# Performance work log

Hardware: AMD Instinct MI355X
Metric: run time of the kernel (lower is better)

Reference implementation:

```python
import jax, jax.numpy as jnp
import numpy as np

N = 4096   # query tokens
M = 4096   # key/value tokens
D = 512    # embedding_dim


def setup_inputs() -> dict:
    key = jax.random.key(0)
    kq, kk, kv = jax.random.split(key, 3)
    return {
        "query": jax.random.normal(kq, (N, D), dtype=jnp.float32),
        "key": jax.random.normal(kk, (M, D), dtype=jnp.float32),
        "value": jax.random.normal(kv, (M, D), dtype=jnp.float32),
    }


def reference(query, key, value):
    # scores = Q K^T  (no 1/sqrt(d) scaling in the original module)
    attention_scores = jnp.einsum("nd,md->nm", query, key)  # [N, M]
    attention_probs = jax.nn.softmax(attention_scores, axis=-1)  # [N, M]
    output = jnp.einsum("nm,md->nd", attention_probs, value)  # [N, D]
    return (output, attention_probs)
```

## Files before the change

kernel.cpp:

```cpp
#include <hip/hip_runtime.h>
#include <hip/hip_bf16.h>
#include <stdint.h>

#define N_Q 4096
#define N_K 4096
#define DIM 512

typedef float f32x4 __attribute__((ext_vector_type(4)));
typedef __bf16 bf16x8 __attribute__((ext_vector_type(8)));
typedef unsigned short u16x4 __attribute__((ext_vector_type(4)));
typedef int i32x4 __attribute__((ext_vector_type(4)));

__device__ __forceinline__ f32x4 mfma_bf16(bf16x8 a, bf16x8 b, f32x4 c) {
  return __builtin_amdgcn_mfma_f32_16x16x32_bf16(a, b, c, 0, 0, 0);
}

__device__ __forceinline__ i32x4 mfma_i8(i32x4 a, i32x4 b, i32x4 c) {
  return __builtin_amdgcn_mfma_i32_16x16x64_i8(a, b, c, 0, 0, 0);
}

__device__ __forceinline__ void gload16(const void* g, void* l) {
  __builtin_amdgcn_global_load_lds((const __attribute__((address_space(1))) void*)g,
                                   (__attribute__((address_space(3))) void*)l,
                                   16, 0, 0);
}

__device__ __forceinline__ void split4(const f32x4 v, u16x4& h, u16x4& l) {
#pragma unroll
  for (int i = 0; i < 4; ++i) {
    float f = v[i];
    uint32_t u = __builtin_bit_cast(uint32_t, f);
    uint32_t hb = (u + 0x8000u) & 0xffff0000u;
    float hf = __builtin_bit_cast(float, hb);
    float lf = f - hf;
    h[i] = (unsigned short)(hb >> 16);
    l[i] = (unsigned short)(__builtin_bit_cast(uint32_t, lf) >> 16);
  }
}

__device__ __forceinline__ unsigned short bf16r(float f) {
  uint32_t u = __builtin_bit_cast(uint32_t, f);
  return (unsigned short)((u + 0x8000u) >> 16);
}

__global__ __launch_bounds__(256) void prep_kernel(const float* __restrict__ Q,
                                                   const float* __restrict__ K,
                                                   const float* __restrict__ V,
                                                   signed char* __restrict__ Xq8,
                                                   signed char* __restrict__ Xk8,
                                                   float* __restrict__ sclA,
                                                   float* __restrict__ sclB,
                                                   unsigned short* __restrict__ Vt) {
  __shared__ unsigned short t[64][72];
  const int bid = blockIdx.x;
  const int tid = threadIdx.x;

  if (bid < 2048) {
    const bool isK = bid >= 1024;
    const float* X = isK ? K : Q;
    signed char* X8 = isK ? Xk8 : Xq8;
    float* scl = isK ? sclB : sclA;
    const int lane = tid & 63;
    const int row = (isK ? bid - 1024 : bid) * 4 + (tid >> 6);

    f32x4 v[2];
    v[0] = *(const f32x4*)(X + (size_t)row * DIM + lane * 8);
    v[1] = *(const f32x4*)(X + (size_t)row * DIM + lane * 8 + 4);

    float mx = 0.f;
#pragma unroll
    for (int u = 0; u < 2; ++u)
#pragma unroll
      for (int j = 0; j < 4; ++j) mx = fmaxf(mx, fabsf(v[u][j]));
#pragma unroll
    for (int o = 32; o > 0; o >>= 1) mx = fmaxf(mx, __shfl_xor(mx, o, 64));

    const float s = fmaxf(mx, 1e-20f) * (1.0f / 127.0f);
    const float rinv = 1.0f / s;
    const float linv = 128.0f * rinv;

    uint32_t hw[2], lw[2];
#pragma unroll
    for (int u = 0; u < 2; ++u) {
      uint32_t hword = 0, lword = 0;
#pragma unroll
      for (int j = 0; j < 4; ++j) {
        float x = v[u][j];
        int h = __float2int_rn(x * rinv);
        float r = x - s * (float)h;
        int l = __float2int_rn(r * linv);
        hword |= ((uint32_t)(h & 0xff)) << (8 * j);
        lword |= ((uint32_t)(l & 0xff)) << (8 * j);
      }
      hw[u] = hword; lw[u] = lword;
    }
    uint2 hv; hv.x = hw[0]; hv.y = hw[1];
    uint2 lv; lv.x = lw[0]; lv.y = lw[1];
    *(uint2*)(X8 + (size_t)row * 1024 + lane * 8) = hv;
    *(uint2*)(X8 + (size_t)row * 1024 + 512 + lane * 8) = lv;
    if (lane == 0) scl[row] = s;
  } else {
    const int b2 = bid - 2048;
    const int d0 = (b2 & 7) * 64;
    const int k0 = (b2 >> 3) * 64;
#pragma unroll
    for (int c = 0; c < 4; ++c) {
      int kr = (tid >> 4) + c * 16;
      f32x4 v = *(const f32x4*)(V + (size_t)(k0 + kr) * DIM + d0 + (tid & 15) * 4);
#pragma unroll
      for (int j = 0; j < 4; ++j) t[(tid & 15) * 4 + j][kr] = bf16r(v[j]);
    }
    __syncthreads();
#pragma unroll
    for (int c = 0; c < 2; ++c) {
      int d = (tid >> 3) + c * 32;
      int k = (tid & 7) * 8;
      *(uint4*)(Vt + (size_t)(d0 + d) * N_K + k0 + k) = *(const uint4*)&t[d][k];
    }
  }
}

__global__ __launch_bounds__(512, 2) void qk5_kernel(const signed char* __restrict__ Xq8,
                                                     const signed char* __restrict__ Xk8,
                                                     const float* __restrict__ sclA,
                                                     const float* __restrict__ sclB,
                                                     float* __restrict__ S) {
  __shared__ __align__(16) char smem[98304];

  const int tid = threadIdx.x;
  const int lane = tid & 63, wid = tid >> 6;
  const int wr = wid >> 1, wc = wid & 1;

  const int bid = blockIdx.x;
  const int b = (bid & 7) * 64 + (bid >> 3);
  const int rbase = (b >> 5) * 256;
  const int cbase = (b & 31) * 128;

  const i32x4 izero = {0, 0, 0, 0};
  i32x4 acc_hh[4][4], acc_x[4][4];
#pragma unroll
  for (int m = 0; m < 4; ++m)
#pragma unroll
    for (int n = 0; n < 4; ++n) { acc_hh[m][n] = izero; acc_x[m][n] = izero; }

  auto stage = [&](int buf, int t) {
    const int rsub = tid >> 3;
    const int sc = (lane & 7) ^ ((lane >> 3) & 7);
    const int colb = (sc < 4) ? (t * 64 + sc * 16) : (512 + t * 64 + (sc & 3) * 16);
#pragma unroll
    for (int i = 0; i < 4; ++i) {
      const int r = i * 64 + rsub;
      const signed char* g = Xq8 + (size_t)(rbase + r) * 1024 + colb;
      uint32_t off = (uint32_t)(buf * 49152 + ((i * 64 + wid * 8) << 7));
      off = (uint32_t)__builtin_amdgcn_readfirstlane((int)off);
      gload16(g, smem + off);
    }
#pragma unroll
    for (int i = 0; i < 2; ++i) {
      const int r = i * 64 + rsub;
      const signed char* g = Xk8 + (size_t)(cbase + r) * 1024 + colb;
      uint32_t off = (uint32_t)(buf * 49152 + 32768 + ((i * 64 + wid * 8) << 7));
      off = (uint32_t)__builtin_amdgcn_readfirstlane((int)off);
      gload16(g, smem + off);
    }
  };

  auto compute = [&](int buf) {
    const char* bA = smem + buf * 49152;
    const char* bB = bA + 32768;
    const int kc = lane >> 4;
    i32x4 ah[4], al[4], bh[4], bl[4];
#pragma unroll
    for (int m = 0; m < 4; ++m) {
      int row = (wr << 6) + (m << 4) + (lane & 15);
      ah[m] = *(const i32x4*)(bA + row * 128 + ((kc ^ (row & 7)) << 4));
      al[m] = *(const i32x4*)(bA + row * 128 + (((4 + kc) ^ (row & 7)) << 4));
    }
#pragma unroll
    for (int n = 0; n < 4; ++n) {
      int row = (wc << 6) + (n << 4) + (lane & 15);
      bh[n] = *(const i32x4*)(bB + row * 128 + ((kc ^ (row & 7)) << 4));
      bl[n] = *(const i32x4*)(bB + row * 128 + (((4 + kc) ^ (row & 7)) << 4));
    }
    __builtin_amdgcn_s_setprio(1);
#pragma unroll
    for (int m = 0; m < 4; ++m)
#pragma unroll
      for (int n = 0; n < 4; ++n) {
        acc_hh[m][n] = mfma_i8(ah[m], bh[n], acc_hh[m][n]);
        acc_x[m][n]  = mfma_i8(ah[m], bl[n], acc_x[m][n]);
        acc_x[m][n]  = mfma_i8(al[m], bh[n], acc_x[m][n]);
      }
    __builtin_amdgcn_s_setprio(0);
  };

  stage(0, 0);
  stage(1, 1);
  for (int t = 0; t < 8; ++t) {
    if (t < 7) asm volatile("s_waitcnt vmcnt(6)" ::: "memory");
    else       asm volatile("s_waitcnt vmcnt(0)" ::: "memory");
    __builtin_amdgcn_s_barrier();
    compute(t & 1);
    asm volatile("s_waitcnt lgkmcnt(0)" ::: "memory");
    __builtin_amdgcn_sched_barrier(0);
    __builtin_amdgcn_s_barrier();
    if (t + 2 < 8) stage(t & 1, t + 2);
  }

#pragma unroll
  for (int m = 0; m < 4; ++m) {
    int row0 = rbase + wr * 64 + m * 16 + (lane >> 4) * 4;
    float sa[4];
#pragma unroll
    for (int j = 0; j < 4; ++j) sa[j] = sclA[row0 + j];
#pragma unroll
    for (int n = 0; n < 4; ++n) {
      int col = cbase + wc * 64 + n * 16 + (lane & 15);
      float sb = sclB[col];
#pragma unroll
      for (int j = 0; j < 4; ++j) {
        float f = (float)acc_hh[m][n][j] + (float)acc_x[m][n][j] * 0.0078125f;
        S[(size_t)(row0 + j) * N_K + col] = sa[j] * sb * f;
      }
    }
  }
}

__global__ __launch_bounds__(256, 2) void qk_kernel(const float* __restrict__ Q,
                                                    const float* __restrict__ K,
                                                    float* __restrict__ S) {
  __shared__ __align__(16) char sAh[16384];
  __shared__ __align__(16) char sAl[16384];
  __shared__ __align__(16) char sBh[16384];
  __shared__ __align__(16) char sBl[16384];

  const int tid = threadIdx.x;
  const int rbase = blockIdx.y * 128;
  const int cbase = blockIdx.x * 128;
  const int lane = tid & 63, wid = tid >> 6;
  const int wr = wid >> 1, wc = wid & 1;
  const int lr = lane & 15, lk = (lane >> 4) * 8;

  const int srow = tid >> 4;
  const int scol = (tid & 15) * 4;

  f32x4 qr[8], kr[8];
#pragma unroll
  for (int p = 0; p < 8; ++p) {
    int r = p * 16 + srow;
    qr[p] = *(const f32x4*)(Q + (size_t)(rbase + r) * DIM + scol);
    kr[p] = *(const f32x4*)(K + (size_t)(cbase + r) * DIM + scol);
  }

  const f32x4 fzero = {0.f, 0.f, 0.f, 0.f};
  f32x4 acc[4][4];
#pragma unroll
  for (int m = 0; m < 4; ++m)
#pragma unroll
    for (int n = 0; n < 4; ++n) acc[m][n] = fzero;

  for (int kk = 0; kk < DIM / 64; ++kk) {
    __syncthreads();
#pragma unroll
    for (int p = 0; p < 8; ++p) {
      int r = p * 16 + srow;
      uint32_t bo = (uint32_t)(r * 128) + (uint32_t)((scol * 2) ^ ((r & 7) << 4));
      u16x4 qh, ql, kh, kl;
      split4(qr[p], qh, ql);
      split4(kr[p], kh, kl);
      *(u16x4*)(sAh + bo) = qh;
      *(u16x4*)(sAl + bo) = ql;
      *(u16x4*)(sBh + bo) = kh;
      *(u16x4*)(sBl + bo) = kl;
    }
    __syncthreads();
    if (kk < DIM / 64 - 1) {
#pragma unroll
      for (int p = 0; p < 8; ++p) {
        int r = p * 16 + srow;
        qr[p] = *(const f32x4*)(Q + (size_t)(rbase + r) * DIM + (kk + 1) * 64 + scol);
        kr[p] = *(const f32x4*)(K + (size_t)(cbase + r) * DIM + (kk + 1) * 64 + scol);
      }
    }
#pragma unroll
    for (int kh = 0; kh < 2; ++kh) {
      bf16x8 a_h[4], a_l[4], b_h[4], b_l[4];
#pragma unroll
      for (int m = 0; m < 4; ++m) {
        int row = wr * 64 + m * 16 + lr;
        uint32_t co = (uint32_t)(((kh * 32 + lk) * 2) ^ ((row & 7) << 4));
        a_h[m] = *(const bf16x8*)(sAh + row * 128 + co);
        a_l[m] = *(const bf16x8*)(sAl + row * 128 + co);
      }
#pragma unroll
      for (int n = 0; n < 4; ++n) {
        int row = wc * 64 + n * 16 + lr;
        uint32_t co = (uint32_t)(((kh * 32 + lk) * 2) ^ ((row & 7) << 4));
        b_h[n] = *(const bf16x8*)(sBh + row * 128 + co);
        b_l[n] = *(const bf16x8*)(sBl + row * 128 + co);
      }
#pragma unroll
      for (int m = 0; m < 4; ++m)
#pragma unroll
        for (int n = 0; n < 4; ++n) {
          acc[m][n] = mfma_bf16(a_h[m], b_h[n], acc[m][n]);
          acc[m][n] = mfma_bf16(a_h[m], b_l[n], acc[m][n]);
          acc[m][n] = mfma_bf16(a_l[m], b_h[n], acc[m][n]);
        }
    }
  }

#pragma unroll
  for (int m = 0; m < 4; ++m) {
    int row = rbase + wr * 64 + m * 16 + (lane >> 4) * 4;
#pragma unroll
    for (int n = 0; n < 4; ++n) {
      int col = cbase + wc * 64 + n * 16 + lr;
#pragma unroll
      for (int j = 0; j < 4; ++j)
        S[(size_t)(row + j) * N_K + col] = acc[m][n][j];
    }
  }
}

__global__ __launch_bounds__(256) void softmax_kernel(float* __restrict__ P,
                                                      unsigned short* __restrict__ Pb) {
  const int tid = threadIdx.x;
  const int wid = tid >> 6, lane = tid & 63;
  float* p = P + (size_t)blockIdx.x * N_K;

  f32x4 v[4];
  float mx = -3.0e38f;
#pragma unroll
  for (int i = 0; i < 4; ++i) {
    v[i] = *(const f32x4*)(p + i * 1024 + tid * 4);
    mx = fmaxf(mx, fmaxf(fmaxf(v[i][0], v[i][1]), fmaxf(v[i][2], v[i][3])));
  }
#pragma unroll
  for (int o = 32; o > 0; o >>= 1) mx = fmaxf(mx, __shfl_xor(mx, o, 64));
  __shared__ float redM[4];
  __shared__ float redS[4];
  if (lane == 0) redM[wid] = mx;
  __syncthreads();
  mx = fmaxf(fmaxf(redM[0], redM[1]), fmaxf(redM[2], redM[3]));

  float s = 0.f;
#pragma unroll
  for (int i = 0; i < 4; ++i) {
#pragma unroll
    for (int j = 0; j < 4; ++j) {
      v[i][j] = __expf(v[i][j] - mx);
      s += v[i][j];
    }
  }
#pragma unroll
  for (int o = 32; o > 0; o >>= 1) s += __shfl_xor(s, o, 64);
  if (lane == 0) redS[wid] = s;
  __syncthreads();
  s = redS[0] + redS[1] + redS[2] + redS[3];
  const float inv = 1.0f / s;

  unsigned short* pb = Pb + (size_t)blockIdx.x * N_K;
#pragma unroll
  for (int i = 0; i < 4; ++i) {
    v[i] *= inv;
    *(f32x4*)(p + i * 1024 + tid * 4) = v[i];
    u16x4 h;
#pragma unroll
    for (int j = 0; j < 4; ++j) h[j] = bf16r(v[i][j]);
    *(u16x4*)(pb + i * 1024 + tid * 4) = h;
  }
}

__global__ __launch_bounds__(256, 2) void pv5_kernel(const unsigned short* __restrict__ Pb,
                                                     const unsigned short* __restrict__ Vt,
                                                     float* __restrict__ Opart) {
  __shared__ __align__(16) char smem[65536];

  const int tid = threadIdx.x;
  const int lane = tid & 63, wid = tid >> 6;
  const int wr = wid >> 1, wc = wid & 1;
  const int rbase = blockIdx.y * 128;
  const int cbase = blockIdx.x * 128;
  const int k0 = blockIdx.z * 1024;
  float* Out = Opart + (size_t)blockIdx.z * ((size_t)N_Q * DIM);

  const int lrow = lane >> 3;
  const int lchk = lane & 7;

  const f32x4 fzero = {0.f, 0.f, 0.f, 0.f};
  f32x4 acc[4][4];
#pragma unroll
  for (int m = 0; m < 4; ++m)
#pragma unroll
    for (int n = 0; n < 4; ++n) acc[m][n] = fzero;

  auto stage = [&](int buf, int t) {
    const size_t kel = (size_t)k0 + ((size_t)t << 6);
#pragma unroll
    for (int i = 0; i < 4; ++i) {
      const int rr = (wid << 5) + (i << 3) + lrow;
      const int gc = lchk ^ (rr & 7);
      const void* gA = (const void*)(Pb + (size_t)(rbase + rr) * N_K + kel + (gc << 3));
      uint32_t off = (uint32_t)(buf * 32768 + (((wid << 5) + (i << 3)) << 7));
      off = (uint32_t)__builtin_amdgcn_readfirstlane((int)off);
      gload16(gA, smem + off);
    }
#pragma unroll
    for (int i = 0; i < 4; ++i) {
      const int rr = (wid << 5) + (i << 3) + lrow;
      const int gc = lchk ^ (rr & 7);
      const void* gB = (const void*)(Vt + (size_t)(cbase + rr) * N_K + kel + (gc << 3));
      uint32_t off = (uint32_t)(buf * 32768 + 16384 + (((wid << 5) + (i << 3)) << 7));
      off = (uint32_t)__builtin_amdgcn_readfirstlane((int)off);
      gload16(gB, smem + off);
    }
  };

  auto compute = [&](int buf) {
    const char* bA = smem + buf * 32768;
    const char* bB = bA + 16384;
#pragma unroll
    for (int kh = 0; kh < 2; ++kh) {
      bf16x8 a[4], bfr[4];
#pragma unroll
      for (int m = 0; m < 4; ++m) {
        int row = (wr << 6) + (m << 4) + (lane & 15);
        uint32_t co = (uint32_t)(((((kh << 2) + (lane >> 4)) << 4)) ^ ((row & 7) << 4));
        a[m] = *(const bf16x8*)(bA + row * 128 + co);
      }
#pragma unroll
      for (int n = 0; n < 4; ++n) {
        int row = (wc << 6) + (n << 4) + (lane & 15);
        uint32_t co = (uint32_t)(((((kh << 2) + (lane >> 4)) << 4)) ^ ((row & 7) << 4));
        bfr[n] = *(const bf16x8*)(bB + row * 128 + co);
      }
      __builtin_amdgcn_s_setprio(1);
#pragma unroll
      for (int m = 0; m < 4; ++m)
#pragma unroll
        for (int n = 0; n < 4; ++n)
          acc[m][n] = mfma_bf16(a[m], bfr[n], acc[m][n]);
      __builtin_amdgcn_s_setprio(0);
    }
  };

  stage(0, 0);
  stage(1, 1);
  for (int t = 0; t < 16; ++t) {
    if (t < 15) asm volatile("s_waitcnt vmcnt(8)" ::: "memory");
    else        asm volatile("s_waitcnt vmcnt(0)" ::: "memory");
    __builtin_amdgcn_s_barrier();
    compute(t & 1);
    asm volatile("s_waitcnt lgkmcnt(0)" ::: "memory");
    __builtin_amdgcn_sched_barrier(0);
    __builtin_amdgcn_s_barrier();
    if (t + 2 < 16) stage(t & 1, t + 2);
  }

#pragma unroll
  for (int m = 0; m < 4; ++m) {
    int row = rbase + wr * 64 + m * 16 + (lane >> 4) * 4;
#pragma unroll
    for (int n = 0; n < 4; ++n) {
      int col = cbase + wc * 64 + n * 16 + (lane & 15);
#pragma unroll
      for (int j = 0; j < 4; ++j)
        Out[(size_t)(row + j) * DIM + col] = acc[m][n][j];
    }
  }
}

__global__ __launch_bounds__(256) void reduce_kernel(float* __restrict__ O,
                                                     const float* __restrict__ Opart) {
  size_t i = ((size_t)blockIdx.x * 256 + threadIdx.x) * 4;
  f32x4 s = *(const f32x4*)(Opart + i);
#pragma unroll
  for (int z = 1; z < 4; ++z)
    s += *(const f32x4*)(Opart + (size_t)z * ((size_t)N_Q * DIM) + i);
  *(f32x4*)(O + i) = s;
}

__global__ __launch_bounds__(256) void softmax_fb_kernel(float* __restrict__ P) {
  const int tid = threadIdx.x;
  const int wid = tid >> 6, lane = tid & 63;
  float* p = P + (size_t)blockIdx.x * N_K;

  f32x4 v[4];
  float mx = -3.0e38f;
#pragma unroll
  for (int i = 0; i < 4; ++i) {
    v[i] = *(const f32x4*)(p + i * 1024 + tid * 4);
    mx = fmaxf(mx, fmaxf(fmaxf(v[i][0], v[i][1]), fmaxf(v[i][2], v[i][3])));
  }
#pragma unroll
  for (int o = 32; o > 0; o >>= 1) mx = fmaxf(mx, __shfl_xor(mx, o, 64));
  __shared__ float redM[4];
  __shared__ float redS[4];
  if (lane == 0) redM[wid] = mx;
  __syncthreads();
  mx = fmaxf(fmaxf(redM[0], redM[1]), fmaxf(redM[2], redM[3]));

  float s = 0.f;
#pragma unroll
  for (int i = 0; i < 4; ++i)
#pragma unroll
    for (int j = 0; j < 4; ++j) {
      v[i][j] = __expf(v[i][j] - mx);
      s += v[i][j];
    }
#pragma unroll
  for (int o = 32; o > 0; o >>= 1) s += __shfl_xor(s, o, 64);
  if (lane == 0) redS[wid] = s;
  __syncthreads();
  s = redS[0] + redS[1] + redS[2] + redS[3];
  const float inv = 1.0f / s;
#pragma unroll
  for (int i = 0; i < 4; ++i) {
    v[i] *= inv;
    *(f32x4*)(p + i * 1024 + tid * 4) = v[i];
  }
}

__global__ __launch_bounds__(512, 2) void pv_kernel(const float* __restrict__ P,
                                                    const float* __restrict__ V,
                                                    float* __restrict__ O) {
  __shared__ __align__(16) char sA[16384];
  __shared__ __align__(16) char sB[16384];

  const int tid = threadIdx.x;
  const int rbase = blockIdx.y * 128;
  const int cbase = blockIdx.x * 128;
  const int lane = tid & 63, wid = tid >> 6;
  const int wr = wid >> 2, wc = wid & 3;
  const int lr = lane & 15, lk = (lane >> 4) * 8;

  const int a_row = tid >> 4;
  const int a_col = (tid & 15) * 4;
  const int b_c = tid & 127;
  const int b_oct = tid >> 7;

  f32x4 areg[4];
  float breg[4][4];
#pragma unroll
  for (int p = 0; p < 4; ++p) {
    int r = p * 32 + a_row;
    areg[p] = *(const f32x4*)(P + (size_t)(rbase + r) * N_K + a_col);
  }
#pragma unroll
  for (int g = 0; g < 4; ++g) {
    int kr0 = b_oct * 4 + g * 16;
#pragma unroll
    for (int i = 0; i < 4; ++i)
      breg[g][i] = V[(size_t)(kr0 + i) * DIM + cbase + b_c];
  }

  const f32x4 fzero = {0.f, 0.f, 0.f, 0.f};
  f32x4 acc[4][2];
#pragma unroll
  for (int m = 0; m < 4; ++m)
#pragma unroll
    for (int n = 0; n < 2; ++n) acc[m][n] = fzero;

  for (int kk = 0; kk < N_K / 64; ++kk) {
    __syncthreads();
#pragma unroll
    for (int p = 0; p < 4; ++p) {
      int r = p * 32 + a_row;
      uint32_t bo = (uint32_t)(r * 128) + (uint32_t)((a_col * 2) ^ ((r & 7) << 4));
      u16x4 hv;
#pragma unroll
      for (int i = 0; i < 4; ++i) hv[i] = bf16r(areg[p][i]);
      *(u16x4*)(sA + bo) = hv;
    }
#pragma unroll
    for (int g = 0; g < 4; ++g) {
      int kr0 = b_oct * 4 + g * 16;
      uint32_t bo = (uint32_t)(b_c * 128) + (uint32_t)((kr0 * 2) ^ ((b_c & 7) << 4));
      u16x4 hv;
#pragma unroll
      for (int i = 0; i < 4; ++i) hv[i] = bf16r(breg[g][i]);
      *(u16x4*)(sB + bo) = hv;
    }
    __syncthreads();
    if (kk < N_K / 64 - 1) {
#pragma unroll
      for (int p = 0; p < 4; ++p) {
        int r = p * 32 + a_row;
        areg[p] = *(const f32x4*)(P + (size_t)(rbase + r) * N_K + (kk + 1) * 64 + a_col);
      }
#pragma unroll
      for (int g = 0; g < 4; ++g) {
        int kr0 = b_oct * 4 + g * 16;
#pragma unroll
        for (int i = 0; i < 4; ++i)
          breg[g][i] = V[(size_t)((kk + 1) * 64 + kr0 + i) * DIM + cbase + b_c];
      }
    }
#pragma unroll
    for (int kh = 0; kh < 2; ++kh) {
      bf16x8 af[4], bf[2];
#pragma unroll
      for (int m = 0; m < 4; ++m) {
        int row = wr * 64 + m * 16 + lr;
        uint32_t co = (uint32_t)(((kh * 32 + lk) * 2) ^ ((row & 7) << 4));
        af[m] = *(const bf16x8*)(sA + row * 128 + co);
      }
#pragma unroll
      for (int n = 0; n < 2; ++n) {
        int row = wc * 32 + n * 16 + lr;
        uint32_t co = (uint32_t)(((kh * 32 + lk) * 2) ^ ((row & 7) << 4));
        bf[n] = *(const bf16x8*)(sB + row * 128 + co);
      }
#pragma unroll
      for (int m = 0; m < 4; ++m)
#pragma unroll
        for (int n = 0; n < 2; ++n)
          acc[m][n] = mfma_bf16(af[m], bf[n], acc[m][n]);
    }
  }

#pragma unroll
  for (int m = 0; m < 4; ++m) {
    int row = rbase + wr * 64 + m * 16 + (lane >> 4) * 4;
#pragma unroll
    for (int n = 0; n < 2; ++n) {
      int col = cbase + wc * 32 + n * 16 + lr;
#pragma unroll
      for (int j = 0; j < 4; ++j)
        O[(size_t)(row + j) * DIM + col] = acc[m][n][j];
    }
  }
}

extern "C" void kernel_launch(void* const* d_in, const int* in_sizes, int n_in,
                              void* d_out, int out_size, void* d_ws, size_t ws_size,
                              hipStream_t stream) {
  const float* Q = (const float*)d_in[0];
  const float* K = (const float*)d_in[1];
  const float* V = (const float*)d_in[2];
  float* O = (float*)d_out;
  float* P = O + (size_t)N_Q * DIM;

  const size_t PB_BYTES = (size_t)N_Q * N_K * 2;
  const size_t VT_BYTES = (size_t)DIM * N_K * 2;
  const size_t SCL_BYTES = 65536;
  const size_t OP_BYTES = (size_t)N_Q * DIM * 4;

  if (ws_size >= PB_BYTES + VT_BYTES + SCL_BYTES + 4 * OP_BYTES) {
    char* wsb = (char*)d_ws;
    signed char* Xq8 = (signed char*)wsb;
    signed char* Xk8 = Xq8 + (size_t)N_Q * 1024;
    unsigned short* Pb = (unsigned short*)wsb;
    unsigned short* Vt = (unsigned short*)(wsb + PB_BYTES);
    float* sclA = (float*)(wsb + PB_BYTES + VT_BYTES);
    float* sclB = sclA + N_Q;
    float* Opart = (float*)(wsb + PB_BYTES + VT_BYTES + SCL_BYTES);

    prep_kernel<<<2560, 256, 0, stream>>>(Q, K, V, Xq8, Xk8, sclA, sclB, Vt);
    qk5_kernel<<<512, 512, 0, stream>>>(Xq8, Xk8, sclA, sclB, P);
    softmax_kernel<<<N_Q, 256, 0, stream>>>(P, Pb);
    pv5_kernel<<<dim3(DIM / 128, N_Q / 128, 4), 256, 0, stream>>>(Pb, Vt, Opart);
    reduce_kernel<<<(N_Q * DIM) / (256 * 4), 256, 0, stream>>>(O, Opart);
  } else {
    qk_kernel<<<dim3(N_K / 128, N_Q / 128), 256, 0, stream>>>(Q, K, P);
    softmax_fb_kernel<<<N_Q, 256, 0, stream>>>(P);
    pv_kernel<<<dim3(DIM / 128, N_Q / 128), 512, 0, stream>>>(P, V, O);
  }
}
```

Measured before the change: 114.2 us.

## Shrink QK int8 tile to 128x128 with triple-buffered interleaved staging

The QK int8 GEMM kernel now uses 128x128 output tiles instead of 256x128, with a 2x4 wave layout and 1024 blocks. Shared memory moves from double to triple buffering of 32KB stages. Global-to-LDS loads for step t+2 are spread across the per-row MFMA loop, which drops the second barrier per iteration. This is meant to cut sync stalls and improve load/compute overlap, at the cost of less data reuse per block and more redundant global reads.

Result: slower. 120.6 us (+5.6%).

```diff
diff --git a/kernel.cpp b/kernel.cpp
--- a/kernel.cpp
+++ b/kernel.cpp
@@ -120,7 +120,7 @@
   }
 }
 
-__global__ __launch_bounds__(512, 2) void qk5_kernel(const signed char* __restrict__ Xq8,
+__global__ __launch_bounds__(512, 2) void qk6_kernel(const signed char* __restrict__ Xq8,
                                                      const signed char* __restrict__ Xk8,
                                                      const float* __restrict__ sclA,
                                                      const float* __restrict__ sclB,
@@ -129,82 +129,72 @@
 
   const int tid = threadIdx.x;
   const int lane = tid & 63, wid = tid >> 6;
-  const int wr = wid >> 1, wc = wid & 1;
+  const int wr = wid >> 2, wc = wid & 3;
 
   const int bid = blockIdx.x;
-  const int b = (bid & 7) * 64 + (bid >> 3);
-  const int rbase = (b >> 5) * 256;
+  const int b = (bid & 7) * 128 + (bid >> 3);
+  const int rbase = (b >> 5) * 128;
   const int cbase = (b & 31) * 128;
 
   const i32x4 izero = {0, 0, 0, 0};
-  i32x4 acc_hh[4][4], acc_x[4][4];
+  i32x4 acc_hh[4][2], acc_x[4][2];
 #pragma unroll
   for (int m = 0; m < 4; ++m)
 #pragma unroll
-    for (int n = 0; n < 4; ++n) { acc_hh[m][n] = izero; acc_x[m][n] = izero; }
-
-  auto stage = [&](int buf, int t) {
-    const int rsub = tid >> 3;
-    const int sc = (lane & 7) ^ ((lane >> 3) & 7);
+    for (int n = 0; n < 2; ++n) { acc_hh[m][n] = izero; acc_x[m][n] = izero; }
+
+  auto stage_unit = [&](int buf, int t, int u) {
+    const int j = u & 1;
+    const int r = j * 64 + (tid >> 3);
+    const int sc = (tid & 7) ^ (r & 7);
     const int colb = (sc < 4) ? (t * 64 + sc * 16) : (512 + t * 64 + (sc & 3) * 16);
-#pragma unroll
-    for (int i = 0; i < 4; ++i) {
-      const int r = i * 64 + rsub;
-      const signed char* g = Xq8 + (size_t)(rbase + r) * 1024 + colb;
-      uint32_t off = (uint32_t)(buf * 49152 + ((i * 64 + wid * 8) << 7));
-      off = (uint32_t)__builtin_amdgcn_readfirstlane((int)off);
-      gload16(g, smem + off);
-    }
-#pragma unroll
-    for (int i = 0; i < 2; ++i) {
-      const int r = i * 64 + rsub;
-      const signed char* g = Xk8 + (size_t)(cbase + r) * 1024 + colb;
-      uint32_t off = (uint32_t)(buf * 49152 + 32768 + ((i * 64 + wid * 8) << 7));
-      off = (uint32_t)__builtin_amdgcn_readfirstlane((int)off);
-      gload16(g, smem + off);
-    }
+    const signed char* g = ((u < 2) ? Xq8 + (size_t)(rbase + r) * 1024
+                                    : Xk8 + (size_t)(cbase + r) * 1024) + colb;
+    uint32_t off = (uint32_t)(buf * 32768 + ((u < 2) ? 0 : 16384) + j * 8192 + wid * 1024);
+    off = (uint32_t)__builtin_amdgcn_readfirstlane((int)off);
+    gload16(g, smem + off);
   };
 
-  auto compute = [&](int buf) {
-    const char* bA = smem + buf * 49152;
-    const char* bB = bA + 32768;
-    const int kc = lane >> 4;
-    i32x4 ah[4], al[4], bh[4], bl[4];
-#pragma unroll
-    for (int m = 0; m < 4; ++m) {
-      int row = (wr << 6) + (m << 4) + (lane & 15);
-      ah[m] = *(const i32x4*)(bA + row * 128 + ((kc ^ (row & 7)) << 4));
-      al[m] = *(const i32x4*)(bA + row * 128 + (((4 + kc) ^ (row & 7)) << 4));
-    }
-#pragma unroll
-    for (int n = 0; n < 4; ++n) {
-      int row = (wc << 6) + (n << 4) + (lane & 15);
+#pragma unroll
+  for (int u = 0; u < 4; ++u) stage_unit(0, 0, u);
+#pragma unroll
+  for (int u = 0; u < 4; ++u) stage_unit(1, 1, u);
+
+  const int kc = lane >> 4;
+  for (int t = 0; t < 8; ++t) {
+    if (t < 7) asm volatile("s_waitcnt vmcnt(4)" ::: "memory");
+    else       asm volatile("s_waitcnt vmcnt(0)" ::: "memory");
+    __builtin_amdgcn_s_barrier();
+    const int cur = t % 3;
+    const int nxt = (t + 2) % 3;
+    const bool st = (t + 2 < 8);
+    const char* bA = smem + cur * 32768;
+    const char* bB = bA + 16384;
+
+    i32x4 bh[2], bl[2];
+#pragma unroll
+    for (int n = 0; n < 2; ++n) {
+      int row = wc * 32 + n * 16 + (lane & 15);
       bh[n] = *(const i32x4*)(bB + row * 128 + ((kc ^ (row & 7)) << 4));
       bl[n] = *(const i32x4*)(bB + row * 128 + (((4 + kc) ^ (row & 7)) << 4));
     }
-    __builtin_amdgcn_s_setprio(1);
-#pragma unroll
-    for (int m = 0; m < 4; ++m)
-#pragma unroll
-      for (int n = 0; n < 4; ++n) {
-        acc_hh[m][n] = mfma_i8(ah[m], bh[n], acc_hh[m][n]);
-        acc_x[m][n]  = mfma_i8(ah[m], bl[n], acc_x[m][n]);
-        acc_x[m][n]  = mfma_i8(al[m], bh[n], acc_x[m][n]);
-      }
-    __builtin_amdgcn_s_setprio(0);
-  };
-
-  stage(0, 0);
-  stage(1, 1);
-  for (int t = 0; t < 8; ++t) {
-    if (t < 7) asm volatile("s_waitcnt vmcnt(6)" ::: "memory");
-    else       asm volatile("s_waitcnt vmcnt(0)" ::: "memory");
-    __builtin_amdgcn_s_barrier();
-    compute(t & 1);
-    asm volatile("s_waitcnt lgkmcnt(0)" ::: "memory");
-    __builtin_amdgcn_sched_barrier(0);
-    __builtin_amdgcn_s_barrier();
-    if (t + 2 < 8) stage(t & 1, t + 2);
+
+#pragma unroll
+    for (int m = 0; m < 4; ++m) {
+      if (st) stage_unit(nxt, t + 2, m);
+      int row = wr * 64 + m * 16 + (lane & 15);
+      i32x4 ah = *(const i32x4*)(bA + row * 128 + ((kc ^ (row & 7)) << 4));
+      i32x4 al = *(const i32x4*)(bA + row * 128 + (((4 + kc) ^ (row & 7)) << 4));
+      __builtin_amdgcn_s_setprio(1);
+#pragma unroll
+      for (int n = 0; n < 2; ++n) {
+        acc_hh[m][n] = mfma_i8(ah, bh[n], acc_hh[m][n]);
+        acc_x[m][n]  = mfma_i8(ah, bl[n], acc_x[m][n]);
+        acc_x[m][n]  = mfma_i8(al, bh[n], acc_x[m][n]);
+      }
+      __builtin_amdgcn_s_setprio(0);
+      __builtin_amdgcn_sched_barrier(0);
+    }
   }
 
 #pragma unroll
@@ -214,8 +204,8 @@
 #pragma unroll
     for (int j = 0; j < 4; ++j) sa[j] = sclA[row0 + j];
 #pragma unroll
-    for (int n = 0; n < 4; ++n) {
-      int col = cbase + wc * 64 + n * 16 + (lane & 15);
+    for (int n = 0; n < 2; ++n) {
+      int col = cbase + wc * 32 + n * 16 + (lane & 15);
       float sb = sclB[col];
 #pragma unroll
       for (int j = 0; j < 4; ++j) {
@@ -658,7 +648,7 @@
     float* Opart = (float*)(wsb + PB_BYTES + VT_BYTES + SCL_BYTES);
 
     prep_kernel<<<2560, 256, 0, stream>>>(Q, K, V, Xq8, Xk8, sclA, sclB, Vt);
-    qk5_kernel<<<512, 512, 0, stream>>>(Xq8, Xk8, sclA, sclB, P);
+    qk6_kernel<<<1024, 512, 0, stream>>>(Xq8, Xk8, sclA, sclB, P);
     softmax_kernel<<<N_Q, 256, 0, stream>>>(P, Pb);
     pv5_kernel<<<dim3(DIM / 128, N_Q / 128, 4), 256, 0, stream>>>(Pb, Vt, Opart);
     reduce_kernel<<<(N_Q * DIM) / (256 * 4), 256, 0, stream>>>(O, Opart);
```
